# Kernel tuning notes

Hardware: AMD Instinct MI355X
Metric: run time of the kernel (lower is better)

## Reference

```python
import jax, jax.numpy as jnp
import numpy as np

N, C, T, V = 16, 128, 128, 25
K, H, OC = 3, 8, 256          # kernel_size subsets, heads, out_channels
HOPMAX = 12                   # hop values in [0, 12); emb_table size HOPMAX
EPS_BN = 1e-5
EPS_NORM = 1e-4


def setup_inputs() -> dict:
    key = jax.random.key(0)
    ks = jax.random.split(key, 12)
    s = 0.05
    x = jax.random.normal(ks[0], (N, C, T, V), jnp.float32)
    hop = jax.random.randint(ks[1], (V, V), 0, HOPMAX)
    emb_table = jax.random.normal(ks[2], (K, H, HOPMAX), jnp.float32) * s
    # A initialized as identity (as in the module) plus small noise for nontrivial grads
    A = jnp.tile(jnp.eye(V, dtype=jnp.float32), (K, H, 1, 1)) \
        + jax.random.normal(ks[3], (K, H, V, V), jnp.float32) * s
    w_block = jax.random.normal(ks[4], (K * OC, C // H), jnp.float32) * s  # grouped 1x1 conv, groups=K*H
    b_block = jax.random.normal(ks[5], (K * OC,), jnp.float32) * s
    bn_gamma = jnp.ones((OC,), jnp.float32)
    bn_beta = jnp.zeros((OC,), jnp.float32)
    res_w = jax.random.normal(ks[6], (OC, C), jnp.float32) * s  # residual 1x1 conv
    res_b = jax.random.normal(ks[7], (OC,), jnp.float32) * s
    res_bn_gamma = jnp.ones((OC,), jnp.float32)
    res_bn_beta = jnp.zeros((OC,), jnp.float32)
    return {"x": x, "hop": hop, "emb_table": emb_table, "A": A,
            "w_block": w_block, "b_block": b_block,
            "bn_gamma": bn_gamma, "bn_beta": bn_beta,
            "res_w": res_w, "res_b": res_b,
            "res_bn_gamma": res_bn_gamma, "res_bn_beta": res_bn_beta}


def _batchnorm(x, gamma, beta):
    # training-mode BatchNorm2d: batch stats over (N, T, V), biased variance
    m = jnp.mean(x, axis=(0, 2, 3), keepdims=True)
    v = jnp.var(x, axis=(0, 2, 3), keepdims=True)
    xn = (x - m) * jax.lax.rsqrt(v + EPS_BN)
    return gamma[None, :, None, None] * xn + beta[None, :, None, None]


def _l2_col_norm(w):
    # torch.norm(w, p=2, dim=-2, keepdim=True) + 1e-4  (in-degree normalization)
    return jnp.sqrt(jnp.sum(w * w, axis=-2, keepdims=True)) + EPS_NORM


def reference(x, hop, emb_table, A, w_block, b_block, bn_gamma, bn_beta,
              res_w, res_b, res_bn_gamma, res_bn_beta):
    n, c, t, v = x.shape
    # residual: 1x1 TemporalConv2d + BN (in_channels != out_channels)
    res = jnp.einsum('nctv,oc->notv', x, res_w) + res_b[None, :, None, None]
    res = _batchnorm(res, res_bn_gamma, res_bn_beta)

    # hop-embedding gather -> [K, H, V, V]; fuse normalized B and A
    B = emb_table[:, :, hop]
    BnA = B / _l2_col_norm(B) + A / _l2_col_norm(A)

    # graph conv: einsum over joint dim v (broadcast over k)
    xh = x.reshape(n, H, c // H, t, v)                      # [N,H,C/H,T,V]
    y = jnp.einsum('nhctv,khvw->nkhctw', xh, BnA)           # [N,K,H,C/H,T,V]
    y = y.reshape(n, K * H, c // H, t, v)                   # groups = K*H

    # grouped 1x1 conv: per-group [C/H -> OC/H] GEMM
    wg = w_block.reshape(K * H, OC // H, c // H)
    out = jnp.einsum('ngctv,goc->ngotv', y, wg)             # [N,K*H,OC/H,T,V]
    out = out.reshape(n, K * OC, t, v) + b_block[None, :, None, None]

    # sum over the K kernel subsets
    out = out.reshape(n, K, OC, t, v).sum(axis=1)
    out = _batchnorm(out, bn_gamma, bn_beta)
    return jax.nn.relu(out + res)
```

## Files before the change

kernel.cpp:

```cpp
#include <hip/hip_runtime.h>
#include <stdint.h>

typedef __attribute__((ext_vector_type(8))) short short8;
typedef __attribute__((ext_vector_type(4))) float f32x4;

#define B_BNA    0ull
#define B_STATS  60416ull
#define B_RESW2  64512ull
#define B_PART   130048ull
#define B_E2     1178624ull
#define B_XB     7994368ull
#define B_MAIN   21625856ull
#define B_RES    47840256ull

#define NTV 51200.0f

__device__ __forceinline__ unsigned short f2bf(float f) {
    unsigned u = __float_as_uint(f);
    return (unsigned short)((u + 0x7fffu + ((u >> 16) & 1u)) >> 16);
}
__device__ __forceinline__ float bf2f(unsigned s) { return __uint_as_float(s << 16); }

__device__ __forceinline__ float wave_sum(float v) {
#pragma unroll
    for (int m = 1; m < 64; m <<= 1) v += __shfl_xor(v, m, 64);
    return v;
}

__device__ __forceinline__ void gl_lds16(const unsigned short* g, unsigned short* l) {
    __builtin_amdgcn_global_load_lds(
        (const __attribute__((address_space(1))) unsigned int*)g,
        (__attribute__((address_space(3))) unsigned int*)l, 16, 0, 0);
}

__global__ __launch_bounds__(256) void k_prep(const int* __restrict__ hop,
                                              const float* __restrict__ emb,
                                              const float* __restrict__ A,
                                              const float* __restrict__ res_w,
                                              float* __restrict__ bna,
                                              float* __restrict__ stats,
                                              unsigned short* __restrict__ resw2) {
    int g = blockIdx.x, tid = threadIdx.x;
    if (g < 24) {
        if (tid < 25) {
            int w = tid;
            float nb = 0.f, na = 0.f;
            for (int v = 0; v < 25; v++) {
                float e = emb[g*12 + hop[v*25 + w]];
                nb += e*e;
                float a = A[((size_t)g*25 + v)*25 + w];
                na += a*a;
            }
            nb = sqrtf(nb) + 1e-4f;
            na = sqrtf(na) + 1e-4f;
            for (int v = 0; v < 25; v++) {
                float e = emb[g*12 + hop[v*25 + w]];
                float a = A[((size_t)g*25 + v)*25 + w];
                bna[g*625 + v*25 + w] = e/nb + a/na;
            }
        }
    } else if (g == 24) {
#pragma unroll
        for (int i = 0; i < 4; i++) stats[i*256 + tid] = 0.f;
    } else {
        int base = (g - 25) * 4096 + tid * 16;
#pragma unroll
        for (int j = 0; j < 16; j++) resw2[base + j] = f2bf(res_w[base + j]);
    }
}

__global__ __launch_bounds__(256) void k_prep2x(const float* __restrict__ w_block,
                                                const float* __restrict__ bna,
                                                unsigned short* __restrict__ E2,
                                                const float* __restrict__ x,
                                                unsigned short* __restrict__ xb) {
    int bid = blockIdx.x, tid = threadIdx.x;
    if (bid < 128) {
        __shared__ float bl[3*625];
        __shared__ float wl[3*64];
        int half = bid & 1, og = (bid >> 1) & 7, h = bid >> 4;

        for (int i = tid; i < 1875; i += 256) {
            int k3 = i / 625, j = i - k3*625;
            bl[i] = bna[(k3*8 + h)*625 + j];
        }
        if (tid < 192) {
            int k3 = tid >> 6, o = (tid >> 4) & 3, c = tid & 15;
            wl[tid] = w_block[(k3*256 + h*32 + og*4 + o)*16 + c];
        }
        __syncthreads();

        unsigned short* dst = E2 + (size_t)(h*8 + og)*53248;
        int e0 = half * 26624;
        for (int e = e0 + tid; e < e0 + 26624; e += 256) {
            int kc = e >> 12;
            int n  = (e >> 5) & 127;
            int kk = e & 31;
            int k  = kc*32 + kk;
            int o  = n >> 5, w = n & 31;
            float val = 0.f;
            if (k < 400 && w < 25) {
                int c = k / 25, v = k - c*25;
                val = wl[0*64 + o*16 + c] * bl[0*625 + v*25 + w]
                    + wl[1*64 + o*16 + c] * bl[1*625 + v*25 + w]
                    + wl[2*64 + o*16 + c] * bl[2*625 + v*25 + w];
            }
            dst[e] = f2bf(val);
        }
    } else {
        int b = bid - 128;
        int n_ = b >> 7, t_ = b & 127;
        unsigned short* row = xb + (size_t)b * 3328;
        for (int idx = tid; idx < 3200; idx += 256) {
            int c = idx / 25, v = idx - c*25;
            float val = x[(((size_t)n_*128 + c)*128 + t_)*25 + v];
            row[(c >> 4)*416 + (c & 15)*25 + v] = f2bf(val);
        }
        if (tid < 128) row[(tid >> 4)*416 + 400 + (tid & 15)] = 0;
    }
}

__global__ __launch_bounds__(256) void k_mm(const unsigned short* __restrict__ xb,
                                            const unsigned short* __restrict__ E2,
                                            unsigned short* __restrict__ mainp,
                                            const float* __restrict__ x,
                                            const unsigned short* __restrict__ resw2,
                                            unsigned short* __restrict__ resp,
                                            float* __restrict__ stats) {
    __shared__ unsigned short Alds[128*32];
    __shared__ unsigned short Blds[128*32];
    int bid = blockIdx.x, tid = threadIdx.x;
    int lane = tid & 63, wave = tid >> 6;
    int wm = wave >> 1, wn = wave & 1;
    int lane15 = lane & 15, quad = lane >> 4;

    if (bid < 1024) {
        int h = bid & 7, og = (bid >> 3) & 7, mt = bid >> 6;

        const unsigned short* ag = xb + (size_t)(mt*128 + wave*32 + (lane>>2))*3328
                                      + h*416 + (lane&3)*8;
        const unsigned short* bg = E2 + (size_t)(h*8 + og)*53248 + wave*1024 + lane*8;
        unsigned short* al = &Alds[wave*1024 + lane*8];
        unsigned short* bl = &Blds[wave*1024 + lane*8];

        f32x4 acc[4][4] = {};

        for (int kc = 0; kc < 13; kc++) {
            gl_lds16(ag,          al);
            gl_lds16(ag + 53248,  al + 512);
            gl_lds16(bg,          bl);
            gl_lds16(bg + 512,    bl + 512);
            ag += 32; bg += 4096;
            __syncthreads();

            short8 af[4], bf[4];
#pragma unroll
            for (int i = 0; i < 4; i++) {
                af[i] = *(const short8*)&Alds[(wm*64 + i*16 + lane15)*32 + quad*8];
                bf[i] = *(const short8*)&Blds[(wn*64 + i*16 + lane15)*32 + quad*8];
            }
#pragma unroll
            for (int i = 0; i < 4; i++)
#pragma unroll
                for (int j = 0; j < 4; j++)
                    acc[i][j] = __builtin_amdgcn_mfma_f32_16x16x32_bf16(af[i], bf[j], acc[i][j], 0, 0, 0);
            __syncthreads();
        }

        float s1[2] = {0.f, 0.f}, s2[2] = {0.f, 0.f};
#pragma unroll
        for (int j = 0; j < 4; j++) {
            int w = (j & 1)*16 + lane15;
            int p = j >> 1;
            if (w < 25) {
                int oc = h*32 + og*4 + wn*2 + p;
#pragma unroll
                for (int i = 0; i < 4; i++) {
                    int mb = mt*128 + wm*64 + i*16 + quad*4;
#pragma unroll
                    for (int r = 0; r < 4; r++) {
                        float val = acc[i][j][r];
                        mainp[(size_t)((mb + r)*256 + oc)*25 + w] = f2bf(val);
                        s1[p] += val;
                        s2[p] = fmaf(val, val, s2[p]);
                    }
                }
            }
        }
#pragma unroll
        for (int p = 0; p < 2; p++) {
            float a = wave_sum(s1[p]);
            float b = wave_sum(s2[p]);
            if (lane == 0) {
                int oc = h*32 + og*4 + wn*2 + p;
                atomicAdd(&stats[oc], a);
                atomicAdd(&stats[256 + oc], b);
            }
        }
    } else {
        int b2 = bid - 1024;
        int nt = (b2 >= 400) ? 1 : 0;
        int mt = b2 - nt*400;

        int m2row = tid >> 1, shalf = tid & 1;
        int m2 = mt*128 + m2row;
        int bb = m2 / 25, vv = m2 - bb*25;
        int n_ = bb >> 7, t_ = bb & 127;
        const float* xbase = x + ((size_t)n_*128*128 + t_)*25 + vv;

        const unsigned short* rbg = resw2 + (size_t)(nt*128 + wave*32 + (lane>>2))*128
                                          + (lane&3)*8;
        unsigned short* bl = &Blds[wave*1024 + lane*8];

        f32x4 acc[4][4] = {};

        for (int kc = 0; kc < 4; kc++) {
            {
                unsigned short tmp[16];
                int c0 = kc*32 + shalf*16;
#pragma unroll
                for (int j = 0; j < 16; j++)
                    tmp[j] = f2bf(xbase[(size_t)(c0 + j)*3200]);
                unsigned pk[8];
#pragma unroll
                for (int q = 0; q < 8; q++)
                    pk[q] = (unsigned)tmp[2*q] | ((unsigned)tmp[2*q+1] << 16);
                *(uint4*)&Alds[m2row*32 + shalf*16]     = make_uint4(pk[0], pk[1], pk[2], pk[3]);
                *(uint4*)&Alds[m2row*32 + shalf*16 + 8] = make_uint4(pk[4], pk[5], pk[6], pk[7]);
            }
            gl_lds16(rbg + kc*32,        bl);
            gl_lds16(rbg + 2048 + kc*32, bl + 512);
            __syncthreads();

            short8 af[4], bf[4];
#pragma unroll
            for (int i = 0; i < 4; i++) {
                af[i] = *(const short8*)&Alds[(wm*64 + i*16 + lane15)*32 + quad*8];
                bf[i] = *(const short8*)&Blds[(wn*64 + i*16 + lane15)*32 + quad*8];
            }
#pragma unroll
            for (int i = 0; i < 4; i++)
#pragma unroll
                for (int j = 0; j < 4; j++)
                    acc[i][j] = __builtin_amdgcn_mfma_f32_16x16x32_bf16(af[i], bf[j], acc[i][j], 0, 0, 0);
            __syncthreads();
        }

#pragma unroll
        for (int j = 0; j < 4; j++) {
            int oc = nt*128 + wn*64 + j*16 + lane15;
            float s1 = 0.f, s2 = 0.f;
#pragma unroll
            for (int i = 0; i < 4; i++) {
                int m2b = mt*128 + wm*64 + i*16 + quad*4;
#pragma unroll
                for (int r = 0; r < 4; r++) {
                    float val = acc[i][j][r];
                    int m2e = m2b + r;
                    int b = m2e / 25, v = m2e - b*25;
                    resp[(size_t)(b*256 + oc)*25 + v] = f2bf(val);
                    s1 += val;
                    s2 = fmaf(val, val, s2);
                }
            }
            s1 += __shfl_xor(s1, 16, 64); s1 += __shfl_xor(s1, 32, 64);
            s2 += __shfl_xor(s2, 16, 64); s2 += __shfl_xor(s2, 32, 64);
            if (quad == 0) {
                atomicAdd(&stats[512 + oc], s1);
                atomicAdd(&stats[768 + oc], s2);
            }
        }
    }
}

__global__ __launch_bounds__(256) void k_final(const float* __restrict__ bn_g,
                                               const float* __restrict__ bn_b,
                                               const float* __restrict__ rbn_g,
                                               const float* __restrict__ rbn_b,
                                               const float* __restrict__ stats,
                                               const unsigned short* __restrict__ mainp,
                                               const unsigned short* __restrict__ resp,
                                               float* __restrict__ out) {
    int b = blockIdx.x;
    int n_ = b >> 7, t_ = b & 127;
    int oc = threadIdx.x;
    const float inv = 1.f / NTV;
    float s1 = stats[oc],       s2 = stats[256 + oc];
    float r1 = stats[512 + oc], r2 = stats[768 + oc];
    float mm = s1*inv, vm = s2*inv - mm*mm;
    float mr = r1*inv, vr = r2*inv - mr*mr;
    float a1 = bn_g[oc]  * rsqrtf(vm + 1e-5f); float c1 = bn_b[oc]  - a1*mm;
    float a2 = rbn_g[oc] * rsqrtf(vr + 1e-5f); float c2 = rbn_b[oc] - a2*mr;

    const unsigned short* mrow = mainp + (size_t)(b*256 + oc)*25;
    const unsigned short* rrow = resp  + (size_t)(b*256 + oc)*25;
    float* op = out + ((size_t)(n_*256 + oc)*128 + t_)*25;
#pragma unroll
    for (int w = 0; w < 25; w++) {
        float val = fmaf(a1, bf2f(mrow[w]), c1) + fmaf(a2, bf2f(rrow[w]), c2);
        op[w] = fmaxf(val, 0.f);
    }
}

extern "C" void kernel_launch(void* const* d_in, const int* in_sizes, int n_in,
                              void* d_out, int out_size, void* d_ws, size_t ws_size,
                              hipStream_t stream) {
    const float* x        = (const float*)d_in[0];
    const int*   hop      = (const int*)  d_in[1];
    const float* emb      = (const float*)d_in[2];
    const float* A        = (const float*)d_in[3];
    const float* w_block  = (const float*)d_in[4];
    const float* bn_g     = (const float*)d_in[6];
    const float* bn_b     = (const float*)d_in[7];
    const float* res_w    = (const float*)d_in[8];
    const float* rbn_g    = (const float*)d_in[10];
    const float* rbn_b    = (const float*)d_in[11];
    float* out = (float*)d_out;

    char* ws = (char*)d_ws;
    float*          bna    = (float*)(ws + B_BNA);
    float*          stats  = (float*)(ws + B_STATS);
    unsigned short* resw2  = (unsigned short*)(ws + B_RESW2);
    unsigned short* E2     = (unsigned short*)(ws + B_E2);
    unsigned short* xb     = (unsigned short*)(ws + B_XB);
    unsigned short* mainp  = (unsigned short*)(ws + B_MAIN);
    unsigned short* resp   = (unsigned short*)(ws + B_RES);

    k_prep   <<<33,   256, 0, stream>>>(hop, emb, A, res_w, bna, stats, resw2);
    k_prep2x <<<2176, 256, 0, stream>>>(w_block, bna, E2, x, xb);
    k_mm     <<<1824, 256, 0, stream>>>(xb, E2, mainp, x, resw2, resp, stats);
    k_final  <<<2048, 256, 0, stream>>>(bn_g, bn_b, rbn_g, rbn_b, stats, mainp, resp, out);
}
```

Before: 232.7 us.

## Double-buffer LDS staging with swizzled layout and coalesced residual x loads

The main GEMM branch now double-buffers its LDS tiles, prefetching the next K-chunk with global_load_lds while MFMAs run on the current one, and drops one barrier per iteration. Both branches use an XOR-swizzled LDS layout to cut bank conflicts on the short8 fragment reads. The residual branch is rewritten so a warp reads contiguous spatial positions of x, making the loads coalesced instead of strided per channel. This doubles the LDS footprint, which may lower occupancy.

After: 222.5 us. 4.4% less time.

```diff
diff --git a/kernel.cpp b/kernel.cpp
--- a/kernel.cpp
+++ b/kernel.cpp
@@ -7,7 +7,6 @@
 #define B_BNA    0ull
 #define B_STATS  60416ull
 #define B_RESW2  64512ull
-#define B_PART   130048ull
 #define B_E2     1178624ull
 #define B_XB     7994368ull
 #define B_MAIN   21625856ull
@@ -31,6 +30,16 @@
     __builtin_amdgcn_global_load_lds(
         (const __attribute__((address_space(1))) unsigned int*)g,
         (__attribute__((address_space(3))) unsigned int*)l, 16, 0, 0);
+}
+__device__ __forceinline__ void stage_pair(const unsigned short* g0, const unsigned short* g1,
+                                           unsigned short* d) {
+    gl_lds16(g0, d);
+    gl_lds16(g1, d + 512);
+}
+
+__device__ __forceinline__ int swz_idx(int row, int quad) {
+    int rowX = row ^ ((row >> 2) & 1);
+    return rowX * 32 + ((quad ^ (row & 3)) << 3);
 }
 
 __global__ __launch_bounds__(256) void k_prep(const int* __restrict__ hop,
@@ -127,44 +136,58 @@
                                             const unsigned short* __restrict__ resw2,
                                             unsigned short* __restrict__ resp,
                                             float* __restrict__ stats) {
-    __shared__ unsigned short Alds[128*32];
-    __shared__ unsigned short Blds[128*32];
+    __shared__ unsigned short lds[16384];
     int bid = blockIdx.x, tid = threadIdx.x;
     int lane = tid & 63, wave = tid >> 6;
     int wm = wave >> 1, wn = wave & 1;
     int lane15 = lane & 15, quad = lane >> 4;
 
+    int Lrow0 = wave*32 + (lane >> 2), Lq = lane & 3;
+    int r0 = Lrow0 ^ ((Lrow0 >> 2) & 1), q0 = Lq ^ (r0 & 3);
+    int Lrow1 = Lrow0 + 16;
+    int r1 = Lrow1 ^ ((Lrow1 >> 2) & 1), q1 = Lq ^ (r1 & 3);
+
+    unsigned short* Ad = lds        + wave*1024 + lane*8;
+    unsigned short* Bd = lds + 4096 + wave*1024 + lane*8;
+
     if (bid < 1024) {
         int h = bid & 7, og = (bid >> 3) & 7, mt = bid >> 6;
 
-        const unsigned short* ag = xb + (size_t)(mt*128 + wave*32 + (lane>>2))*3328
-                                      + h*416 + (lane&3)*8;
-        const unsigned short* bg = E2 + (size_t)(h*8 + og)*53248 + wave*1024 + lane*8;
-        unsigned short* al = &Alds[wave*1024 + lane*8];
-        unsigned short* bl = &Blds[wave*1024 + lane*8];
+        const unsigned short* agA0 = xb + (size_t)(mt*128 + r0)*3328 + h*416 + q0*8;
+        const unsigned short* agA1 = xb + (size_t)(mt*128 + r1)*3328 + h*416 + q1*8;
+        const unsigned short* eb   = E2 + (size_t)(h*8 + og)*53248;
+        const unsigned short* bgB0 = eb + r0*32 + q0*8;
+        const unsigned short* bgB1 = eb + r1*32 + q1*8;
 
         f32x4 acc[4][4] = {};
 
+        stage_pair(agA0, agA1, Ad);
+        stage_pair(bgB0, bgB1, Bd);
+        __syncthreads();
+
         for (int kc = 0; kc < 13; kc++) {
-            gl_lds16(ag,          al);
-            gl_lds16(ag + 53248,  al + 512);
-            gl_lds16(bg,          bl);
-            gl_lds16(bg + 512,    bl + 512);
-            ag += 32; bg += 4096;
-            __syncthreads();
-
-            short8 af[4], bf[4];
+            int cur = (kc & 1) << 13;
+            if (kc < 12) {
+                int nxt = 8192 - cur;
+                stage_pair(agA0 + (kc+1)*32,            agA1 + (kc+1)*32,            Ad + nxt);
+                stage_pair(bgB0 + (size_t)(kc+1)*4096,  bgB1 + (size_t)(kc+1)*4096,  Bd + nxt);
+                __builtin_amdgcn_sched_barrier(0);
+            }
+            const unsigned short* Ac = lds + cur;
+            const unsigned short* Bc = lds + 4096 + cur;
+
+            short8 af[4], bq[4];
 #pragma unroll
             for (int i = 0; i < 4; i++) {
-                af[i] = *(const short8*)&Alds[(wm*64 + i*16 + lane15)*32 + quad*8];
-                bf[i] = *(const short8*)&Blds[(wn*64 + i*16 + lane15)*32 + quad*8];
+                af[i] = *(const short8*)&Ac[swz_idx(wm*64 + i*16 + lane15, quad)];
+                bq[i] = *(const short8*)&Bc[swz_idx(wn*64 + i*16 + lane15, quad)];
             }
 #pragma unroll
             for (int i = 0; i < 4; i++)
 #pragma unroll
                 for (int j = 0; j < 4; j++)
-                    acc[i][j] = __builtin_amdgcn_mfma_f32_16x16x32_bf16(af[i], bf[j], acc[i][j], 0, 0, 0);
-            __syncthreads();
+                    acc[i][j] = __builtin_amdgcn_mfma_f32_16x16x32_bf16(af[i], bq[j], acc[i][j], 0, 0, 0);
+            if (kc < 12) __syncthreads();
         }
 
         float s1[2] = {0.f, 0.f}, s2[2] = {0.f, 0.f};
@@ -202,47 +225,41 @@
         int nt = (b2 >= 400) ? 1 : 0;
         int mt = b2 - nt*400;
 
-        int m2row = tid >> 1, shalf = tid & 1;
-        int m2 = mt*128 + m2row;
-        int bb = m2 / 25, vv = m2 - bb*25;
-        int n_ = bb >> 7, t_ = bb & 127;
-        const float* xbase = x + ((size_t)n_*128*128 + t_)*25 + vv;
-
-        const unsigned short* rbg = resw2 + (size_t)(nt*128 + wave*32 + (lane>>2))*128
-                                          + (lane&3)*8;
-        unsigned short* bl = &Blds[wave*1024 + lane*8];
+        int n  = mt / 25;
+        int off = (mt - n*25) * 128;
+        const float* xb2 = x + (size_t)n*409600 + off;
+
+        int c2 = tid >> 4, seg = tid & 15;
+
+        const unsigned short* rb0 = resw2 + (size_t)(nt*128 + r0)*128 + q0*8;
+        const unsigned short* rb1 = resw2 + (size_t)(nt*128 + r1)*128 + q1*8;
 
         f32x4 acc[4][4] = {};
 
         for (int kc = 0; kc < 4; kc++) {
-            {
-                unsigned short tmp[16];
-                int c0 = kc*32 + shalf*16;
-#pragma unroll
-                for (int j = 0; j < 16; j++)
-                    tmp[j] = f2bf(xbase[(size_t)(c0 + j)*3200]);
-                unsigned pk[8];
-#pragma unroll
-                for (int q = 0; q < 8; q++)
-                    pk[q] = (unsigned)tmp[2*q] | ((unsigned)tmp[2*q+1] << 16);
-                *(uint4*)&Alds[m2row*32 + shalf*16]     = make_uint4(pk[0], pk[1], pk[2], pk[3]);
-                *(uint4*)&Alds[m2row*32 + shalf*16 + 8] = make_uint4(pk[4], pk[5], pk[6], pk[7]);
-            }
-            gl_lds16(rbg + kc*32,        bl);
-            gl_lds16(rbg + 2048 + kc*32, bl + 512);
+            stage_pair(rb0 + kc*32, rb1 + kc*32, Bd);
+            const float* xc0 = xb2 + (size_t)(kc*32 + 2*c2)*3200;
+            const float* xc1 = xc0 + 3200;
+            int wbase = 2*(c2 & 3), qn = c2 >> 2;
+#pragma unroll
+            for (int j = 0; j < 8; j++) {
+                int m = seg + 16*j;
+                unsigned pk = (unsigned)f2bf(xc0[m]) | ((unsigned)f2bf(xc1[m]) << 16);
+                *(unsigned*)&lds[swz_idx(m, qn) + wbase] = pk;
+            }
             __syncthreads();
 
-            short8 af[4], bf[4];
+            short8 af[4], bq[4];
 #pragma unroll
             for (int i = 0; i < 4; i++) {
-                af[i] = *(const short8*)&Alds[(wm*64 + i*16 + lane15)*32 + quad*8];
-                bf[i] = *(const short8*)&Blds[(wn*64 + i*16 + lane15)*32 + quad*8];
+                af[i] = *(const short8*)&lds[swz_idx(wm*64 + i*16 + lane15, quad)];
+                bq[i] = *(const short8*)&lds[4096 + swz_idx(wn*64 + i*16 + lane15, quad)];
             }
 #pragma unroll
             for (int i = 0; i < 4; i++)
 #pragma unroll
                 for (int j = 0; j < 4; j++)
-                    acc[i][j] = __builtin_amdgcn_mfma_f32_16x16x32_bf16(af[i], bf[j], acc[i][j], 0, 0, 0);
+                    acc[i][j] = __builtin_amdgcn_mfma_f32_16x16x32_bf16(af[i], bq[j], acc[i][j], 0, 0, 0);
             __syncthreads();
         }
 
```
